# Performance work log

Measured on AMD Instinct MI355X. Metric: run time of the kernel, lower is better.

The kernel has to match this reference:

```python
import jax, jax.numpy as jnp
import numpy as np

N = 100000   # nodes
E = 1600000  # edges
FEAT = 128
HID = 128
TGT = 64
L = 3
G = 512      # graphs in batch


def setup_inputs() -> dict:
    key = jax.random.key(0)
    ks = jax.random.split(key, 16)
    s = 0.05
    return {
        "x": jax.random.normal(ks[0], (N, FEAT), jnp.float32),
        "edge_index": jax.random.randint(ks[1], (2, E), 0, N, dtype=jnp.int32),
        "batch": jnp.sort(jax.random.randint(ks[2], (N,), 0, G, dtype=jnp.int32)),
        "conv_w1": jax.random.normal(ks[3], (L, FEAT, HID), jnp.float32) * s,
        "conv_b1": jax.random.normal(ks[4], (L, HID), jnp.float32) * s,
        "conv_w2": jax.random.normal(ks[5], (L, HID, HID), jnp.float32) * s,
        "conv_b2": jax.random.normal(ks[6], (L, HID), jnp.float32) * s,
        "eps": jnp.zeros((L,), jnp.float32),
        "gn_scale": jnp.ones((L, HID), jnp.float32),
        "gn_weight": jnp.ones((L, HID), jnp.float32),
        "gn_bias": jnp.zeros((L, HID), jnp.float32),
        "proj_w1": jax.random.normal(ks[7], (L, HID, HID), jnp.float32) * s,
        "proj_b1": jax.random.normal(ks[8], (L, HID), jnp.float32) * s,
        "proj_w2": jax.random.normal(ks[9], (L, HID, TGT), jnp.float32) * s,
        "proj_b2": jax.random.normal(ks[10], (L, TGT), jnp.float32) * s,
    }


def _graph_norm(h, batch, counts, scale, weight, bias):
    # per-graph mean -> scatter back to nodes
    mean = jax.ops.segment_sum(h, batch, num_segments=G) / counts
    sub = h - mean[batch] * scale
    var = jax.ops.segment_sum(sub * sub, batch, num_segments=G) / counts
    std = jnp.sqrt(var + 1e-8)
    return weight * sub / std[batch] + bias


def reference(x, edge_index, batch, conv_w1, conv_b1, conv_w2, conv_b2, eps,
              gn_scale, gn_weight, gn_bias, proj_w1, proj_b1, proj_w2, proj_b2):
    src, dst = edge_index[0], edge_index[1]
    counts = jnp.maximum(
        jax.ops.segment_sum(jnp.ones((N, 1), x.dtype), batch, num_segments=G), 1.0)
    h = x
    z_cat = []
    for l in range(L):
        # GINConv: aggr_j->i then 2-layer MLP
        aggr = jax.ops.segment_sum(h[src], dst, num_segments=N)
        h = (1.0 + eps[l]) * h + aggr
        h = jax.nn.relu(h @ conv_w1[l] + conv_b1[l]) @ conv_w2[l] + conv_b2[l]
        # GraphNorm
        h = _graph_norm(h, batch, counts, gn_scale[l], gn_weight[l], gn_bias[l])
        h = jax.nn.relu(h)
        # projection MLP + global add pool
        z = jax.nn.relu(h @ proj_w1[l] + proj_b1[l]) @ proj_w2[l] + proj_b2[l]
        z_cat.append(jax.ops.segment_sum(z, batch, num_segments=G))
    return jnp.concatenate(z_cat, axis=-1)  # [G, L*TGT]
```

## Files before the change

### kernel.cpp

```cpp
#include <hip/hip_runtime.h>

#define NN 100000
#define EE 1600000
#define HIDD 128
#define TGTT 64
#define GGG 512
#define NBK 98
#define CAPB 17408
#define ABLK 800
#define EPB 2000
#define CVT2 512
#define LSTR 136
#define GBLK 782
#define OUTB 128

typedef unsigned short ushort_t;
typedef __attribute__((ext_vector_type(8))) short short8;
typedef __attribute__((ext_vector_type(4))) float f32x4;
typedef __attribute__((ext_vector_type(4))) unsigned short us4;

__device__ __forceinline__ float b2f(ushort_t u) {
    union { unsigned int i; float f; } v; v.i = ((unsigned int)u) << 16; return v.f;
}
__device__ __forceinline__ ushort_t f2b(float f) {
    union { float f; unsigned int i; } v; v.f = f;
    unsigned int r = (v.i + 0x7fffu + ((v.i >> 16) & 1u)) >> 16;
    return (ushort_t)r;
}

__global__ __launch_bounds__(256) void k_pro(const float* __restrict__ x, ushort_t* __restrict__ Xb,
                                             const float* __restrict__ cw1, const float* __restrict__ cw2,
                                             const float* __restrict__ pw1, ushort_t* __restrict__ Wt,
                                             const int* __restrict__ batch, int* __restrict__ goff,
                                             const int* __restrict__ ei, int* __restrict__ gcnt,
                                             unsigned int* __restrict__ bbuf) {
    __shared__ int cnt[NBK], base[NBK], cur[NBK];
    int b = blockIdx.x, t = threadIdx.x;

    if (b < ABLK) {
        if (t < NBK) cnt[t] = 0;
        __syncthreads();
        int e0 = b * EPB;
        int e1 = min(e0 + EPB, EE);
        for (int e = e0 + t; e < e1; e += 256)
            atomicAdd(&cnt[ei[EE + e] >> 10], 1);
        __syncthreads();
        if (t < NBK) { base[t] = atomicAdd(&gcnt[t], cnt[t]); cur[t] = 0; }
        __syncthreads();
        for (int e = e0 + t; e < e1; e += 256) {
            int s = ei[e], d = ei[EE + e];
            int bk = d >> 10;
            int off = base[bk] + atomicAdd(&cur[bk], 1);
            if (off < CAPB)
                bbuf[(long)bk * CAPB + off] = (unsigned int)s | (((unsigned int)d & 1023u) << 17);
        }
        return;
    }
    b -= ABLK;
    if (b < CVT2) {
        long total = (long)NN * HIDD / 4;
        long step = (long)CVT2 * 256;
        for (long i = (long)b * 256 + t; i < total; i += step) {
            float4 v = ((const float4*)x)[i];
            us4 o; o.x = f2b(v.x); o.y = f2b(v.y); o.z = f2b(v.z); o.w = f2b(v.w);
            ((us4*)Xb)[i] = o;
        }
        return;
    }
    b -= CVT2;
    if (b < 9) {
        int l = b / 3, j = b % 3;
        const float* src = (j == 0 ? cw1 : j == 1 ? cw2 : pw1) + (size_t)l * HIDD * HIDD;
        ushort_t* dst = Wt + (size_t)b * HIDD * HIDD;
        for (int i = t; i < HIDD * HIDD; i += 256)
            dst[(i & 127) * HIDD + (i >> 7)] = f2b(src[i]);
        return;
    }
    b -= 9;
    {
        int g = b * 256 + t;
        if (g > GGG) return;
        int lo = 0, hi = NN;
        while (lo < hi) { int mid = (lo + hi) >> 1; if (batch[mid] < g) lo = mid + 1; else hi = mid; }
        goff[g] = lo;
    }
}

__global__ __launch_bounds__(1024) void k_csr(const int* __restrict__ gcnt,
                                              const unsigned int* __restrict__ bbuf,
                                              int* __restrict__ rowptr, int* __restrict__ csr) {
    __shared__ int ldeg[1024], tsum[1024], sb[NBK];
    int b = blockIdx.x, t = threadIdx.x;
    if (t < NBK) sb[t] = gcnt[t];
    ldeg[t] = 0;
    __syncthreads();
    if (t == 0) { int a = 0; for (int i = 0; i < NBK; i++) { int v = sb[i]; sb[i] = a; a += v; } }
    __syncthreads();
    int cnt = min(gcnt[b], CAPB);
    int base = sb[b];
    const unsigned int* bb = bbuf + (long)b * CAPB;
    for (int i = t; i < cnt; i += 1024) atomicAdd(&ldeg[bb[i] >> 17], 1);
    __syncthreads();
    int d0 = ldeg[t];
    tsum[t] = d0;
    __syncthreads();
    for (int off = 1; off < 1024; off <<= 1) {
        int u = (t >= off) ? tsum[t - off] : 0;
        __syncthreads();
        tsum[t] += u;
        __syncthreads();
    }
    int p0 = base + tsum[t] - d0;
    int gnode = b * 1024 + t;
    if (gnode < NN) rowptr[gnode] = p0;
    if (b == NBK - 1 && t == 0) rowptr[NN] = EE;
    ldeg[t] = p0;
    __syncthreads();
    for (int i = t; i < cnt; i += 1024) {
        unsigned int en = bb[i];
        int pos = atomicAdd(&ldeg[en >> 17], 1);
        csr[pos] = (int)(en & 0x1FFFFu);
    }
}

__global__ __launch_bounds__(256) void k_gmlp(const ushort_t* __restrict__ hin,
                                              const int* __restrict__ rowptr,
                                              const int* __restrict__ csr,
                                              const int* __restrict__ batch,
                                              const float* __restrict__ eps, int l,
                                              const ushort_t* __restrict__ Wt1, const float* __restrict__ B1,
                                              const ushort_t* __restrict__ Wt2, const float* __restrict__ B2,
                                              ushort_t* __restrict__ Y,
                                              float* __restrict__ gsum, float* __restrict__ gsq,
                                              const float* __restrict__ pooledP, const int* __restrict__ goff,
                                              const float* __restrict__ WoP, const float* __restrict__ BoP,
                                              float* __restrict__ outP, int lprev) {
    __shared__ ushort_t sX[128 * LSTR];
    __shared__ int sgid[128];
    int tid = threadIdx.x;

    if (blockIdx.x >= GBLK) {
        if (lprev < 0) return;
        int ob = blockIdx.x - GBLK;
        int sub = tid >> 6, tt = tid & 63;
        int g = ob * 4 + sub;
        if (g >= GGG) return;
        float cntg = (float)(goff[g + 1] - goff[g]);
        float acc = cntg * BoP[tt];
        const float* p = pooledP + (long)g * HIDD;
        for (int k = 0; k < HIDD; k++) acc += p[k] * WoP[k * TGTT + tt];
        outP[(long)g * (3 * TGTT) + lprev * TGTT + tt] = acc;
        return;
    }

    long base = (long)blockIdx.x * 128;
    int lane = tid & 15, ng = tid >> 4;
    int off = lane << 3;
    float e1 = 1.0f + eps[l];

    if (tid < 128) sgid[tid] = (base + tid < NN) ? batch[base + tid] : -1;

#pragma unroll 1
    for (int it = 0; it < 8; it++) {
        int row = it * 16 + ng;
        long node = base + row;
        short8 o = (short8)0;
        if (node < NN) {
            short8 h = *(const short8*)(hin + (node << 7) + off);
            float acc[8];
#pragma unroll
            for (int t = 0; t < 8; t++) acc[t] = e1 * b2f((ushort_t)h[t]);
            int jb = rowptr[node], je = rowptr[node + 1];
            int j = jb;
            for (; j + 8 <= je; j += 8) {
                int s0 = csr[j], s1 = csr[j + 1], s2 = csr[j + 2], s3 = csr[j + 3];
                int s4 = csr[j + 4], s5 = csr[j + 5], s6 = csr[j + 6], s7 = csr[j + 7];
                short8 v0 = *(const short8*)(hin + ((long)s0 << 7) + off);
                short8 v1 = *(const short8*)(hin + ((long)s1 << 7) + off);
                short8 v2 = *(const short8*)(hin + ((long)s2 << 7) + off);
                short8 v3 = *(const short8*)(hin + ((long)s3 << 7) + off);
                short8 v4 = *(const short8*)(hin + ((long)s4 << 7) + off);
                short8 v5 = *(const short8*)(hin + ((long)s5 << 7) + off);
                short8 v6 = *(const short8*)(hin + ((long)s6 << 7) + off);
                short8 v7 = *(const short8*)(hin + ((long)s7 << 7) + off);
#pragma unroll
                for (int t = 0; t < 8; t++)
                    acc[t] += ((b2f((ushort_t)v0[t]) + b2f((ushort_t)v1[t])) +
                               (b2f((ushort_t)v2[t]) + b2f((ushort_t)v3[t]))) +
                              ((b2f((ushort_t)v4[t]) + b2f((ushort_t)v5[t])) +
                               (b2f((ushort_t)v6[t]) + b2f((ushort_t)v7[t])));
            }
            for (; j + 4 <= je; j += 4) {
                int s0 = csr[j], s1 = csr[j + 1], s2 = csr[j + 2], s3 = csr[j + 3];
                short8 v0 = *(const short8*)(hin + ((long)s0 << 7) + off);
                short8 v1 = *(const short8*)(hin + ((long)s1 << 7) + off);
                short8 v2 = *(const short8*)(hin + ((long)s2 << 7) + off);
                short8 v3 = *(const short8*)(hin + ((long)s3 << 7) + off);
#pragma unroll
                for (int t = 0; t < 8; t++)
                    acc[t] += (b2f((ushort_t)v0[t]) + b2f((ushort_t)v1[t])) +
                              (b2f((ushort_t)v2[t]) + b2f((ushort_t)v3[t]));
            }
            for (; j < je; j++) {
                int s = csr[j];
                short8 v = *(const short8*)(hin + ((long)s << 7) + off);
#pragma unroll
                for (int t = 0; t < 8; t++) acc[t] += b2f((ushort_t)v[t]);
            }
#pragma unroll
            for (int t = 0; t < 8; t++) o[t] = (short)f2b(acc[t]);
        }
        *(short8*)(sX + row * LSTR + off) = o;
    }
    __syncthreads();

    int w = tid >> 6, l64 = tid & 63, q = l64 >> 4, l16 = l64 & 15;
    int r0 = w * 16, r1 = 64 + w * 16;
    short8 a0[4], a1[4];
#pragma unroll
    for (int c = 0; c < 4; c++) {
        a0[c] = *(const short8*)(sX + (r0 + l16) * LSTR + q * 8 + c * 32);
        a1[c] = *(const short8*)(sX + (r1 + l16) * LSTR + q * 8 + c * 32);
    }
    f32x4 acc0[8], acc1[8];
#pragma unroll
    for (int nt = 0; nt < 8; nt++) {
        int col = nt * 16 + l16;
        float bias = B1[col];
        f32x4 c0 = {bias, bias, bias, bias};
        f32x4 c1 = c0;
        const ushort_t* bB = Wt1 + col * HIDD + q * 8;
#pragma unroll
        for (int c = 0; c < 4; c++) {
            short8 b = *(const short8*)(bB + c * 32);
            c0 = __builtin_amdgcn_mfma_f32_16x16x32_bf16(a0[c], b, c0, 0, 0, 0);
            c1 = __builtin_amdgcn_mfma_f32_16x16x32_bf16(a1[c], b, c1, 0, 0, 0);
        }
        acc0[nt] = c0; acc1[nt] = c1;
    }
#pragma unroll
    for (int nt = 0; nt < 8; nt++) {
        int col = nt * 16 + l16;
#pragma unroll
        for (int r = 0; r < 4; r++) {
            sX[(r0 + q * 4 + r) * LSTR + col] = f2b(fmaxf(acc0[nt][r], 0.f));
            sX[(r1 + q * 4 + r) * LSTR + col] = f2b(fmaxf(acc1[nt][r], 0.f));
        }
    }
#pragma unroll
    for (int c = 0; c < 4; c++) {
        a0[c] = *(const short8*)(sX + (r0 + l16) * LSTR + q * 8 + c * 32);
        a1[c] = *(const short8*)(sX + (r1 + l16) * LSTR + q * 8 + c * 32);
    }
#pragma unroll
    for (int nt = 0; nt < 8; nt++) {
        int col = nt * 16 + l16;
        float bias = B2[col];
        f32x4 c0 = {bias, bias, bias, bias};
        f32x4 c1 = c0;
        const ushort_t* bB = Wt2 + col * HIDD + q * 8;
#pragma unroll
        for (int c = 0; c < 4; c++) {
            short8 b = *(const short8*)(bB + c * 32);
            c0 = __builtin_amdgcn_mfma_f32_16x16x32_bf16(a0[c], b, c0, 0, 0, 0);
            c1 = __builtin_amdgcn_mfma_f32_16x16x32_bf16(a1[c], b, c1, 0, 0, 0);
        }
#pragma unroll
        for (int r = 0; r < 4; r++) {
            long row0 = base + r0 + q * 4 + r;
            long row1 = base + r1 + q * 4 + r;
            ushort_t h0 = f2b(c0[r]), h1 = f2b(c1[r]);
            if (row0 < NN) Y[(row0 << 7) + col] = h0;
            if (row1 < NN) Y[(row1 << 7) + col] = h1;
            sX[(r0 + q * 4 + r) * LSTR + col] = h0;
            sX[(r1 + q * 4 + r) * LSTR + col] = h1;
        }
    }
    __syncthreads();

    int f = tid & 127, half = tid >> 7;
    int rbeg = half * 64, rend = rbeg + 64;
    float s1 = 0.f, s2 = 0.f;
    int curg = -1;
    for (int row = rbeg; row < rend; row++) {
        int g = sgid[row];
        if (g != curg) {
            if (curg >= 0) {
                atomicAdd(&gsum[(long)curg * HIDD + f], s1);
                atomicAdd(&gsq[(long)curg * HIDD + f], s2);
            }
            s1 = 0.f; s2 = 0.f; curg = g;
        }
        if (g >= 0) { float a = b2f(sX[row * LSTR + f]); s1 += a; s2 += a * a; }
    }
    if (curg >= 0) {
        atomicAdd(&gsum[(long)curg * HIDD + f], s1);
        atomicAdd(&gsq[(long)curg * HIDD + f], s2);
    }
}

__global__ __launch_bounds__(256) void k_projpool(const ushort_t* __restrict__ Hraw,
                                                  const int* __restrict__ batch,
                                                  const float* __restrict__ gsum, const float* __restrict__ gsq,
                                                  const int* __restrict__ goff,
                                                  const float* __restrict__ scale, const float* __restrict__ weight,
                                                  const float* __restrict__ gnbp,
                                                  const ushort_t* __restrict__ Wt, const float* __restrict__ B,
                                                  ushort_t* __restrict__ Hn, float* __restrict__ pooled,
                                                  int store_hn) {
    __shared__ ushort_t sX[128 * LSTR];
    __shared__ int sgid[128];
    __shared__ float sA[4][128], sB[4][128];
    int tid = threadIdx.x;
    long base = (long)blockIdx.x * 128;

    if (tid < 128) sgid[tid] = (base + tid < NN) ? batch[base + tid] : -1;
    __syncthreads();
    int gmin = sgid[0];
    {
        int f = tid & 127;
#pragma unroll
        for (int s = tid >> 7; s < 4; s += 2) {
            int gg = gmin + s;
            if (gg < GGG) {
                float cntg = (float)max(goff[gg + 1] - goff[gg], 1);
                long i = (long)gg * HIDD + f;
                float mean = gsum[i] / cntg;
                float ms = mean * scale[f];
                float var = gsq[i] / cntg - 2.f * ms * mean + ms * ms;
                float A = weight[f] / sqrtf(var + 1e-8f);
                sA[s][f] = A;
                sB[s][f] = gnbp[f] - ms * A;
            }
        }
    }
    __syncthreads();

#pragma unroll
    for (int c = 0; c < 8; c++) {
        int idx = c * 256 + tid;
        int row = idx >> 4, cw = idx & 15;
        long grow = base + row;
        short8 v = (short8)0;
        if (grow < NN) {
            short8 raw = *(const short8*)(Hraw + (grow << 7) + (cw << 3));
            int slot = sgid[row] - gmin;
            const float* pA = &sA[slot][cw << 3];
            const float* pB = &sB[slot][cw << 3];
#pragma unroll
            for (int t = 0; t < 8; t++) {
                float val = b2f((ushort_t)raw[t]) * pA[t] + pB[t];
                v[t] = (short)f2b(val > 0.f ? val : 0.f);
            }
            if (store_hn) *(short8*)(Hn + (grow << 7) + (cw << 3)) = v;
        }
        *(short8*)(sX + row * LSTR + (cw << 3)) = v;
    }
    __syncthreads();

    int w = tid >> 6, l64 = tid & 63, q = l64 >> 4, l16 = l64 & 15;
    int r0 = w * 16, r1 = 64 + w * 16;
    short8 a0[4], a1[4];
#pragma unroll
    for (int c = 0; c < 4; c++) {
        a0[c] = *(const short8*)(sX + (r0 + l16) * LSTR + q * 8 + c * 32);
        a1[c] = *(const short8*)(sX + (r1 + l16) * LSTR + q * 8 + c * 32);
    }
    f32x4 acc0[8], acc1[8];
#pragma unroll
    for (int nt = 0; nt < 8; nt++) {
        int col = nt * 16 + l16;
        float bias = B[col];
        f32x4 c0 = {bias, bias, bias, bias};
        f32x4 c1 = c0;
        const ushort_t* bB = Wt + col * HIDD + q * 8;
#pragma unroll
        for (int c = 0; c < 4; c++) {
            short8 b = *(const short8*)(bB + c * 32);
            c0 = __builtin_amdgcn_mfma_f32_16x16x32_bf16(a0[c], b, c0, 0, 0, 0);
            c1 = __builtin_amdgcn_mfma_f32_16x16x32_bf16(a1[c], b, c1, 0, 0, 0);
        }
        acc0[nt] = c0; acc1[nt] = c1;
    }
#pragma unroll
    for (int nt = 0; nt < 8; nt++) {
        int col = nt * 16 + l16;
#pragma unroll
        for (int r = 0; r < 4; r++) {
            sX[(r0 + q * 4 + r) * LSTR + col] = f2b(fmaxf(acc0[nt][r], 0.f));
            sX[(r1 + q * 4 + r) * LSTR + col] = f2b(fmaxf(acc1[nt][r], 0.f));
        }
    }
    __syncthreads();

    int f = tid & 127, half = tid >> 7;
    int rbeg = half * 64, rend = rbeg + 64;
    float sum = 0.f;
    int curg = -1;
    for (int row = rbeg; row < rend; row++) {
        int g = sgid[row];
        if (g != curg) {
            if (curg >= 0) atomicAdd(&pooled[(long)curg * HIDD + f], sum);
            sum = 0.f; curg = g;
        }
        if (g >= 0) sum += b2f(sX[row * LSTR + f]);
    }
    if (curg >= 0) atomicAdd(&pooled[(long)curg * HIDD + f], sum);
}

__global__ __launch_bounds__(256) void k_out(const float* __restrict__ pooled, const int* __restrict__ goff,
                                             const float* __restrict__ W, const float* __restrict__ B,
                                             float* __restrict__ out, int l) {
    int sub = threadIdx.x >> 6, tt = threadIdx.x & 63;
    int g = blockIdx.x * 4 + sub;
    if (g >= GGG) return;
    float cnt = (float)(goff[g + 1] - goff[g]);
    float acc = cnt * B[tt];
    const float* p = pooled + (long)g * HIDD;
    for (int k = 0; k < HIDD; k++) acc += p[k] * W[k * TGTT + tt];
    out[(long)g * (3 * TGTT) + l * TGTT + tt] = acc;
}

extern "C" void kernel_launch(void* const* d_in, const int* in_sizes, int n_in,
                              void* d_out, int out_size, void* d_ws, size_t ws_size,
                              hipStream_t stream) {
    const float* x    = (const float*)d_in[0];
    const int*   ei   = (const int*)d_in[1];
    const int*   batch= (const int*)d_in[2];
    const float* cw1  = (const float*)d_in[3];
    const float* cb1  = (const float*)d_in[4];
    const float* cw2  = (const float*)d_in[5];
    const float* cb2  = (const float*)d_in[6];
    const float* eps  = (const float*)d_in[7];
    const float* gsc  = (const float*)d_in[8];
    const float* gw   = (const float*)d_in[9];
    const float* gb   = (const float*)d_in[10];
    const float* pw1  = (const float*)d_in[11];
    const float* pb1  = (const float*)d_in[12];
    const float* pw2  = (const float*)d_in[13];
    const float* pb2  = (const float*)d_in[14];
    float* out = (float*)d_out;

    ushort_t* Xb   = (ushort_t*)d_ws;
    ushort_t* Hn   = Xb;
    ushort_t* Hraw = Xb + (size_t)NN * HIDD;
    ushort_t* Wt   = Hraw + (size_t)NN * HIDD;
    float* Ab_unused = (float*)(Wt + (size_t)9 * HIDD * HIDD);
    float* Bb_unused = Ab_unused + (size_t)GGG * HIDD;
    float* pooled_unused = Bb_unused + (size_t)GGG * HIDD;
    int* goff   = (int*)(pooled_unused + (size_t)GGG * HIDD);
    int* rowptr = goff + (GGG + 1);
    int* gcnt   = rowptr + (NN + 1);
    int* csr    = gcnt + NBK;
    unsigned int* bbuf = (unsigned int*)(csr + EE);
    float* acc3 = (float*)bbuf;
    const size_t R = (size_t)GGG * HIDD;

    hipMemsetAsync(gcnt, 0, NBK * sizeof(int), stream);
    k_pro<<<ABLK + CVT2 + 9 + 3, 256, 0, stream>>>(x, Xb, cw1, cw2, pw1, Wt, batch, goff, ei, gcnt, bbuf);
    k_csr<<<NBK, 1024, 0, stream>>>(gcnt, bbuf, rowptr, csr);
    hipMemsetAsync(acc3, 0, 9 * R * sizeof(float), stream);

    for (int l = 0; l < 3; l++) {
        const ushort_t* hin = (l == 0) ? Xb : Hn;
        ushort_t* Wt1 = Wt + (size_t)(l * 3 + 0) * HIDD * HIDD;
        ushort_t* Wt2 = Wt + (size_t)(l * 3 + 1) * HIDD * HIDD;
        ushort_t* Wtp = Wt + (size_t)(l * 3 + 2) * HIDD * HIDD;
        float* gsum_l   = acc3 + (size_t)l * R;
        float* gsq_l    = acc3 + (size_t)(3 + l) * R;
        float* pooled_l = acc3 + (size_t)(6 + l) * R;
        const float* pooled_prev = acc3 + (size_t)(6 + (l > 0 ? l - 1 : 0)) * R;
        int grid = GBLK + (l > 0 ? OUTB : 0);
        k_gmlp<<<grid, 256, 0, stream>>>(hin, rowptr, csr, batch, eps, l,
                                         Wt1, cb1 + l * HIDD, Wt2, cb2 + l * HIDD, Hraw,
                                         gsum_l, gsq_l,
                                         pooled_prev, goff,
                                         pw2 + (size_t)(l - 1) * HIDD * TGTT, pb2 + (l - 1) * TGTT,
                                         out, l - 1);
        k_projpool<<<GBLK, 256, 0, stream>>>(Hraw, batch, gsum_l, gsq_l, goff,
                                             gsc + l * HIDD, gw + l * HIDD, gb + l * HIDD,
                                             Wtp, pb1 + l * HIDD, Hn, pooled_l, (l < 2) ? 1 : 0);
    }
    k_out<<<OUTB, 256, 0, stream>>>(acc3 + (size_t)(6 + 2) * R, goff,
                                    pw2 + (size_t)2 * HIDD * TGTT, pb2 + 2 * TGTT, out, 2);
}
```

Baseline: 582.7 us.

## Build CSR via global degree count, scan, and atomic scatter

Replaces the two-pass bucketed CSR build (per-block LDS bucketing into a staging buffer, then a per-bucket local sort) with a classic global approach: atomic degree counting per destination node, a two-kernel prefix scan to form rowptr and cursors, and a scatter using global atomics on per-node cursors. This removes the staging buffer, its capacity limit and the LDS-heavy k_csr pass. In exchange it adds two kernel launches and relies on many scattered global atomics, and the CSR neighbour order within a row becomes nondeterministic.

```diff
diff --git a/kernel.cpp b/kernel.cpp
--- a/kernel.cpp
+++ b/kernel.cpp
@@ -6,9 +6,8 @@
 #define TGTT 64
 #define GGG 512
 #define NBK 98
-#define CAPB 17408
-#define ABLK 800
-#define EPB 2000
+#define DEGB 512
+#define SCATB 800
 #define CVT2 512
 #define LSTR 136
 #define GBLK 782
@@ -32,31 +31,9 @@
                                              const float* __restrict__ cw1, const float* __restrict__ cw2,
                                              const float* __restrict__ pw1, ushort_t* __restrict__ Wt,
                                              const int* __restrict__ batch, int* __restrict__ goff,
-                                             const int* __restrict__ ei, int* __restrict__ gcnt,
-                                             unsigned int* __restrict__ bbuf) {
-    __shared__ int cnt[NBK], base[NBK], cur[NBK];
+                                             const int* __restrict__ ei, int* __restrict__ deg) {
     int b = blockIdx.x, t = threadIdx.x;
 
-    if (b < ABLK) {
-        if (t < NBK) cnt[t] = 0;
-        __syncthreads();
-        int e0 = b * EPB;
-        int e1 = min(e0 + EPB, EE);
-        for (int e = e0 + t; e < e1; e += 256)
-            atomicAdd(&cnt[ei[EE + e] >> 10], 1);
-        __syncthreads();
-        if (t < NBK) { base[t] = atomicAdd(&gcnt[t], cnt[t]); cur[t] = 0; }
-        __syncthreads();
-        for (int e = e0 + t; e < e1; e += 256) {
-            int s = ei[e], d = ei[EE + e];
-            int bk = d >> 10;
-            int off = base[bk] + atomicAdd(&cur[bk], 1);
-            if (off < CAPB)
-                bbuf[(long)bk * CAPB + off] = (unsigned int)s | (((unsigned int)d & 1023u) << 17);
-        }
-        return;
-    }
-    b -= ABLK;
     if (b < CVT2) {
         long total = (long)NN * HIDD / 4;
         long step = (long)CVT2 * 256;
@@ -68,6 +45,13 @@
         return;
     }
     b -= CVT2;
+    if (b < DEGB) {
+        long step = (long)DEGB * 256;
+        for (long e = (long)b * 256 + t; e < EE; e += step)
+            atomicAdd(&deg[ei[EE + e]], 1);
+        return;
+    }
+    b -= DEGB;
     if (b < 9) {
         int l = b / 3, j = b % 3;
         const float* src = (j == 0 ? cw1 : j == 1 ? cw2 : pw1) + (size_t)l * HIDD * HIDD;
@@ -86,22 +70,29 @@
     }
 }
 
-__global__ __launch_bounds__(1024) void k_csr(const int* __restrict__ gcnt,
-                                              const unsigned int* __restrict__ bbuf,
-                                              int* __restrict__ rowptr, int* __restrict__ csr) {
-    __shared__ int ldeg[1024], tsum[1024], sb[NBK];
+__global__ __launch_bounds__(1024) void k_rp1(const int* __restrict__ deg, int* __restrict__ bsum) {
+    __shared__ int red[1024];
     int b = blockIdx.x, t = threadIdx.x;
-    if (t < NBK) sb[t] = gcnt[t];
-    ldeg[t] = 0;
+    int gnode = b * 1024 + t;
+    red[t] = (gnode < NN) ? deg[gnode] : 0;
+    __syncthreads();
+    for (int off = 512; off > 0; off >>= 1) {
+        if (t < off) red[t] += red[t + off];
+        __syncthreads();
+    }
+    if (t == 0) bsum[b] = red[0];
+}
+
+__global__ __launch_bounds__(1024) void k_rp2(const int* __restrict__ deg, const int* __restrict__ bsum,
+                                              int* __restrict__ rowptr, int* __restrict__ cursor) {
+    __shared__ int sb[NBK], tsum[1024];
+    int b = blockIdx.x, t = threadIdx.x;
+    if (t < NBK) sb[t] = bsum[t];
     __syncthreads();
     if (t == 0) { int a = 0; for (int i = 0; i < NBK; i++) { int v = sb[i]; sb[i] = a; a += v; } }
     __syncthreads();
-    int cnt = min(gcnt[b], CAPB);
-    int base = sb[b];
-    const unsigned int* bb = bbuf + (long)b * CAPB;
-    for (int i = t; i < cnt; i += 1024) atomicAdd(&ldeg[bb[i] >> 17], 1);
-    __syncthreads();
-    int d0 = ldeg[t];
+    int gnode = b * 1024 + t;
+    int d0 = (gnode < NN) ? deg[gnode] : 0;
     tsum[t] = d0;
     __syncthreads();
     for (int off = 1; off < 1024; off <<= 1) {
@@ -110,16 +101,18 @@
         tsum[t] += u;
         __syncthreads();
     }
-    int p0 = base + tsum[t] - d0;
-    int gnode = b * 1024 + t;
-    if (gnode < NN) rowptr[gnode] = p0;
+    int p0 = sb[b] + tsum[t] - d0;
+    if (gnode < NN) { rowptr[gnode] = p0; cursor[gnode] = p0; }
     if (b == NBK - 1 && t == 0) rowptr[NN] = EE;
-    ldeg[t] = p0;
-    __syncthreads();
-    for (int i = t; i < cnt; i += 1024) {
-        unsigned int en = bb[i];
-        int pos = atomicAdd(&ldeg[en >> 17], 1);
-        csr[pos] = (int)(en & 0x1FFFFu);
+}
+
+__global__ __launch_bounds__(256) void k_scat(const int* __restrict__ ei,
+                                              int* __restrict__ cursor, int* __restrict__ csr) {
+    long step = (long)SCATB * 256;
+    for (long e = (long)blockIdx.x * 256 + threadIdx.x; e < EE; e += step) {
+        int s = ei[e], d = ei[EE + e];
+        int pos = atomicAdd(&cursor[d], 1);
+        csr[pos] = s;
     }
 }
 
@@ -450,16 +443,20 @@
     float* pooled_unused = Bb_unused + (size_t)GGG * HIDD;
     int* goff   = (int*)(pooled_unused + (size_t)GGG * HIDD);
     int* rowptr = goff + (GGG + 1);
-    int* gcnt   = rowptr + (NN + 1);
-    int* csr    = gcnt + NBK;
+    int* gcnt_unused = rowptr + (NN + 1);
+    int* csr    = gcnt_unused + NBK;
     unsigned int* bbuf = (unsigned int*)(csr + EE);
     float* acc3 = (float*)bbuf;
     const size_t R = (size_t)GGG * HIDD;
-
-    hipMemsetAsync(gcnt, 0, NBK * sizeof(int), stream);
-    k_pro<<<ABLK + CVT2 + 9 + 3, 256, 0, stream>>>(x, Xb, cw1, cw2, pw1, Wt, batch, goff, ei, gcnt, bbuf);
-    k_csr<<<NBK, 1024, 0, stream>>>(gcnt, bbuf, rowptr, csr);
-    hipMemsetAsync(acc3, 0, 9 * R * sizeof(float), stream);
+    int* deg    = (int*)(acc3 + 9 * R);
+    int* cursor = deg + NN;
+    int* bsum   = cursor + NN;
+
+    hipMemsetAsync(acc3, 0, 9 * R * sizeof(float) + NN * sizeof(int), stream);
+    k_pro<<<CVT2 + DEGB + 9 + 3, 256, 0, stream>>>(x, Xb, cw1, cw2, pw1, Wt, batch, goff, ei, deg);
+    k_rp1<<<NBK, 1024, 0, stream>>>(deg, bsum);
+    k_rp2<<<NBK, 1024, 0, stream>>>(deg, bsum, rowptr, cursor);
+    k_scat<<<SCATB, 256, 0, stream>>>(ei, cursor, csr);
 
     for (int l = 0; l < 3; l++) {
         const ushort_t* hin = (l == 0) ? Xb : Hn;
```

After: 731.5 us. 25.5% more time.
